# Optimization experiments

Hardware: AMD Instinct MI355X
Metric: run time of the kernel (lower is better)

## Reference

```python
import jax, jax.numpy as jnp
import numpy as np

PATCH = 3
PAD = (PATCH - 1) // 2
WEIGHT = 100.0
EPS = 1e-9


def _extract_patches(fm):
    # fm: (C, H, W) -> (H*W, C*9) row i*W+j is the reflect-padded 3x3 patch at (i, j)
    C, H, W = fm.shape
    fm_pad = jnp.pad(fm, ((0, 0), (PAD, PAD), (PAD, PAD)), mode='reflect')
    shifts = [fm_pad[:, dh:dh + H, dw:dw + W] for dh in range(PATCH) for dw in range(PATCH)]
    p = jnp.stack(shifts, axis=0)            # (9, C, H, W)
    return p.reshape(PATCH * PATCH * C, H * W).T  # (HW, 9C)


def _match_fm(content_fm, style_fm):
    # content_fm, style_fm: (1, C, H, W); returns matched style fm (1,C,H,W) and idx (2,H,W)
    C, H, W = content_fm.shape[1:]
    cp = _extract_patches(content_fm[0])     # (HW, 9C) content patches (conv kernels)
    sp = _extract_patches(style_fm[0])       # (HW, 9C) style patches (conv sliding windows)
    c_norm = jnp.sqrt(jnp.sum(cp * cp, axis=1))  # kernel_norm per content location
    s_norm = jnp.sqrt(jnp.sum(sp * sp, axis=1))  # style_fm_norm per style location
    score = cp @ sp.T                            # (HW, HW) cross-correlation
    score = score / (c_norm[:, None] * s_norm[None, :] + EPS)
    idx = jnp.argmax(score, axis=1)              # flat argmax == torch.argmax on (H,W) map
    style_flat = style_fm[0].reshape(C, H * W)
    corr = style_flat[:, idx].reshape(1, C, H, W)  # gather matched style pixels
    corr_idx = jnp.stack([idx // W, idx % W], axis=0).reshape(2, H, W)
    return corr, corr_idx


def _masked_gram(fm, mask_flat, mask_sum):
    # fm: (1, C, H, W), mask_flat: (HW,) -> (C, C) gram of masked fm / sum(mask)
    C = fm.shape[1]
    f = fm[0].reshape(C, -1) * mask_flat[None, :]
    return (f @ f.T) / mask_sum


def setup_inputs() -> dict:
    key = jax.random.key(0)
    k1, k2, k3, k4 = jax.random.split(key, 4)
    B, C, H, W = 1, 512, 64, 64
    return {
        'content_fm': jax.random.normal(k1, (B, C, H, W), dtype=jnp.float32),
        'style_fm': jax.random.normal(k2, (B, C, H, W), dtype=jnp.float32),
        'input_fm': jax.random.normal(k3, (B, C, H, W), dtype=jnp.float32),
        'mask': jax.random.uniform(k4, (B, 1, H, W), dtype=jnp.float32),
    }


def reference(content_fm, style_fm, input_fm, mask):
    H, W = content_fm.shape[2:]
    mask_flat = mask[0, 0].reshape(H * W)
    mask_sum = jnp.sum(mask)
    # capture_style_ref: patch-match style fm to content fm, build target gram
    corr_fm, _ = _match_fm(content_fm, style_fm)
    target_gram = _masked_gram(corr_fm, mask_flat, mask_sum)
    # loss mode: masked gram of current image fm vs target, MSE (mean) * weight
    G = _masked_gram(input_fm, mask_flat, mask_sum)
    loss = jnp.mean((G - target_gram) ** 2) * WEIGHT
    return loss
```

## Files before the change

### kernel.cpp

```cpp
#include <hip/hip_runtime.h>

static constexpr int C  = 512;
static constexpr int P  = 4096;

typedef _Float16 half8  __attribute__((ext_vector_type(8)));
typedef _Float16 half2v __attribute__((ext_vector_type(2)));
typedef float    f32x4  __attribute__((ext_vector_type(4)));

__device__ __forceinline__ int refl(int q) { return q < 0 ? 1 : (q > 63 ? 62 : q); }

__device__ __forceinline__ void g2l16(const void* g, const void* l) {
    __builtin_amdgcn_global_load_lds((const __attribute__((address_space(1))) unsigned int*)g,
                                     (__attribute__((address_space(3))) unsigned int*)l, 16, 0, 0);
}

__global__ __launch_bounds__(256) void k_prep(const float* __restrict__ content, const float* __restrict__ style,
                                              _Float16* __restrict__ Ah, _Float16* __restrict__ Bh,
                                              float* __restrict__ sqn_part) {
    __shared__ float T[64][65];
    __shared__ float R4[4][64];
    const int p0 = (blockIdx.x & 63) * 64, c0 = (blockIdx.x >> 6) * 64;
    const int pl = threadIdx.x & 63, cq = threadIdx.x >> 6;
    const int pv = threadIdx.x >> 3;
    const int cv = (threadIdx.x & 7) * 8;

    #pragma unroll
    for (int r = 0; r < 16; ++r)
        T[cq + r * 4][pl] = content[(size_t)(c0 + cq + r * 4) * P + p0 + pl];
    __syncthreads();
    #pragma unroll
    for (int r = 0; r < 2; ++r) {
        int pl2 = pv + r * 32;
        half8 v;
        #pragma unroll
        for (int u = 0; u < 8; ++u) v[u] = (_Float16)T[cv + u][pl2];
        *(half8*)(Ah + (size_t)(p0 + pl2) * C + c0 + cv) = v;
    }
    __syncthreads();

    float sq = 0.f;
    #pragma unroll
    for (int r = 0; r < 16; ++r) {
        float v = style[(size_t)(c0 + cq + r * 4) * P + p0 + pl];
        T[cq + r * 4][pl] = v;
        sq += v * v;
    }
    R4[cq][pl] = sq;
    __syncthreads();
    if (cq == 0)
        sqn_part[(size_t)(blockIdx.x >> 6) * P + p0 + pl] = R4[0][pl] + R4[1][pl] + R4[2][pl] + R4[3][pl];
    #pragma unroll
    for (int r = 0; r < 2; ++r) {
        int pl2 = pv + r * 32;
        half8 v;
        #pragma unroll
        for (int u = 0; u < 8; ++u) v[u] = (_Float16)T[cv + u][pl2];
        *(half8*)(Bh + (size_t)(p0 + pl2) * C + c0 + cv) = v;
    }
}

__global__ __launch_bounds__(512, 2) void k_gemm16(const _Float16* __restrict__ Ah,
                                                   const _Float16* __restrict__ Bh,
                                                   _Float16* __restrict__ Eo,
                                                   const float* __restrict__ sqn_part,
                                                   const float* __restrict__ mask,
                                                   float* __restrict__ inv_sn,
                                                   float* __restrict__ msum) {
    __shared__ _Float16 SH[65536];
    const int tid = threadIdx.x;
    const int bid = blockIdx.x;
    const int swz = (bid & 7) * 32 + (bid >> 3);
    const int by = swz >> 4, bx = swz & 15;

    if (by == 0) {
        float* sqs = (float*)SH;
        const int b = bx;
        for (int e = tid; e < 384; e += 512) {
            int rr = e >> 6, jw = e & 63;
            int gr = refl(b * 4 - 1 + rr);
            float s = 0.f;
            #pragma unroll
            for (int k = 0; k < 8; ++k) s += sqn_part[(size_t)k * P + gr * 64 + jw];
            sqs[rr * 64 + jw] = s;
        }
        __syncthreads();
        if (tid < 256) {
            int p = b * 256 + tid;
            int li = (tid >> 6) + 1;
            int j = p & 63;
            float s2 = 0.f;
            #pragma unroll
            for (int dh = -1; dh <= 1; ++dh)
                #pragma unroll
                for (int dw = -1; dw <= 1; ++dw)
                    s2 += sqs[(li + dh) * 64 + refl(j + dw)];
            inv_sn[p] = 1.0f / sqrtf(s2);
        }
        if (b == 0) {
            __syncthreads();
            float* red = (float*)SH;
            float s = 0.f;
            for (int e = tid; e < P; e += 512) s += mask[e];
            red[tid] = s;
            __syncthreads();
            for (int t = 256; t > 0; t >>= 1) {
                if (tid < t) red[tid] += red[tid + t];
                __syncthreads();
            }
            if (tid == 0) msum[0] = red[0];
        }
        __syncthreads();
    }

    const int wave = tid >> 6, lane = tid & 63;
    const int wr = wave >> 2, wc = wave & 3;
    const int quad = lane >> 4, l15 = lane & 15;
    const int i0 = by * 256, j0 = bx * 256;

    const int r2 = tid >> 2;
    const int gofs = ((tid & 3) ^ (r2 & 3)) * 8;
    const _Float16* pA0 = Ah + (size_t)(i0 + r2) * C + gofs;
    const _Float16* pA1 = pA0 + (size_t)128 * C;
    const _Float16* pB0 = Bh + (size_t)(j0 + r2) * C + gofs;
    const _Float16* pB1 = pB0 + (size_t)128 * C;
    const int stw0 = wave * 512;
    const int stw1 = 4096 + wave * 512;

    const int aslot = (quad ^ (l15 & 3)) * 8;
    int aoff[8], boff[4];
    #pragma unroll
    for (int mi = 0; mi < 8; ++mi) aoff[mi] = (wr * 128 + mi * 16 + l15) * 32 + aslot;
    #pragma unroll
    for (int ni = 0; ni < 4; ++ni) boff[ni] = (wc * 64 + ni * 16 + l15) * 32 + aslot;

    f32x4 acc[8][4] = {};
    half8 af[8], bf0, bf1, bf2, bf3;

#define LDSA(b,k) (SH + (b) * 16384 + (k) * 8192)
#define LDSB(b,k) (SH + 32768 + (b) * 16384 + (k) * 8192)
#define STAGE_A(b,k,KC) do { g2l16(pA0 + (KC) + (k) * 32, LDSA(b,k) + stw0); \
                             g2l16(pA1 + (KC) + (k) * 32, LDSA(b,k) + stw1); } while (0)
#define STAGE_B(b,k,KC) do { g2l16(pB0 + (KC) + (k) * 32, LDSB(b,k) + stw0); \
                             g2l16(pB1 + (KC) + (k) * 32, LDSB(b,k) + stw1); } while (0)
#define READ_NP0(b,k) do { _Pragma("unroll") for (int mi = 0; mi < 8; ++mi) \
                               af[mi] = *(const half8*)(LDSA(b,k) + aoff[mi]); \
                           bf0 = *(const half8*)(LDSB(b,k) + boff[0]); \
                           bf1 = *(const half8*)(LDSB(b,k) + boff[1]); } while (0)
#define READ_NP1(b,k) do { bf2 = *(const half8*)(LDSB(b,k) + boff[2]); \
                           bf3 = *(const half8*)(LDSB(b,k) + boff[3]); } while (0)
#define MF8(BF,NI) do { _Pragma("unroll") for (int mi = 0; mi < 8; ++mi) \
    acc[mi][NI] = __builtin_amdgcn_mfma_f32_16x16x32_f16(af[mi], BF, acc[mi][NI], 0, 0, 0); } while (0)
#define WAITV4 asm volatile("s_waitcnt vmcnt(4)" ::: "memory")
#define WAITV0 asm volatile("s_waitcnt vmcnt(0)" ::: "memory")
#define EXEC16(B0,N0,B1,N1) do { \
    __builtin_amdgcn_s_barrier(); \
    asm volatile("s_waitcnt lgkmcnt(0)" ::: "memory"); \
    __builtin_amdgcn_sched_barrier(0); \
    __builtin_amdgcn_s_setprio(1); \
    MF8(B0, N0); MF8(B1, N1); \
    __builtin_amdgcn_s_setprio(0); \
    __builtin_amdgcn_s_barrier(); } while (0)

    STAGE_A(0, 0, 0); STAGE_B(0, 0, 0); STAGE_A(0, 1, 0); STAGE_B(0, 1, 0);
    WAITV4;
    __builtin_amdgcn_s_barrier();

    for (int it = 0; it < 4; ++it) {
        const int kk = it * 128;
        const bool nl = (it < 3);
        READ_NP0(0, 0); STAGE_A(1, 0, kk + 64);          EXEC16(bf0, 0, bf1, 1);
        READ_NP1(0, 0); STAGE_B(1, 0, kk + 64); WAITV4;  EXEC16(bf2, 2, bf3, 3);
        READ_NP0(0, 1); STAGE_A(1, 1, kk + 64);          EXEC16(bf0, 0, bf1, 1);
        READ_NP1(0, 1); STAGE_B(1, 1, kk + 64); WAITV4;  EXEC16(bf2, 2, bf3, 3);
        READ_NP0(1, 0); if (nl) STAGE_A(0, 0, kk + 128);
        EXEC16(bf0, 0, bf1, 1);
        READ_NP1(1, 0); if (nl) { STAGE_B(0, 0, kk + 128); WAITV4; } else { WAITV0; }
        EXEC16(bf2, 2, bf3, 3);
        READ_NP0(1, 1); if (nl) STAGE_A(0, 1, kk + 128);
        EXEC16(bf0, 0, bf1, 1);
        READ_NP1(1, 1); if (nl) { STAGE_B(0, 1, kk + 128); WAITV4; }
        EXEC16(bf2, 2, bf3, 3);
    }

#undef LDSA
#undef LDSB
#undef STAGE_A
#undef STAGE_B
#undef READ_NP0
#undef READ_NP1
#undef MF8
#undef WAITV4
#undef WAITV0
#undef EXEC16

    __syncthreads();
    #pragma unroll
    for (int h = 0; h < 2; ++h) {
        if (wr == h) {
            #pragma unroll
            for (int mi = 0; mi < 8; ++mi) {
                const int row = mi * 16 + quad * 4;
                #pragma unroll
                for (int ni = 0; ni < 4; ++ni) {
                    const int col = wc * 64 + ni * 16 + l15;
                    #pragma unroll
                    for (int r = 0; r < 4; ++r)
                        SH[(row + r) * 130 + col] = (_Float16)acc[mi][ni][r];
                }
            }
        }
        __syncthreads();
        {
            const int er  = tid >> 2;
            const int c00 = (tid & 3) * 8;
            const int ew  = er & 63;
            const int rm  = (er & 64) | (ew == 0 ? 1 : ew - 1);
            const int rp  = (er & 64) | (ew == 63 ? 62 : ew + 1);
            _Float16* outRow = Eo + (size_t)(i0 + h * 128 + er) * P + j0;
            #pragma unroll
            for (int cc = 0; cc < 256; cc += 32) {
                half8 ev;
                #pragma unroll
                for (int u = 0; u < 8; ++u) {
                    const int c  = c00 + cc + u;
                    const int cw = c & 63;
                    const int cm = (c & ~63) | (cw == 0 ? 1 : cw - 1);
                    const int cp = (c & ~63) | (cw == 63 ? 62 : cw + 1);
                    ev[u] = (_Float16)((float)SH[rm * 130 + cm] + (float)SH[er * 130 + c] + (float)SH[rp * 130 + cp]);
                }
                *(half8*)(outRow + c00 + cc) = ev;
            }
        }
        if (h == 0) __syncthreads();
    }
}

__global__ __launch_bounds__(256) void k_argmax(const _Float16* __restrict__ E,
                                                const float* __restrict__ inv_sn,
                                                int* __restrict__ idxOut) {
    const int i = blockIdx.x;
    const int ih = i >> 6, iw = i & 63;
    const int wave = threadIdx.x >> 6, l = threadIdx.x & 63, l15 = l & 15;
    size_t rb0 = (size_t)(refl(ih - 1) * 64 + iw) * P;
    size_t rb1 = (size_t)(ih * 64 + iw) * P;
    size_t rb2 = (size_t)(refl(ih + 1) * 64 + iw) * P;

    float best = -1e30f;
    int bidx = 0;
    #pragma unroll
    for (int s = 0; s < 4; ++s) {
        const int j0 = (wave * 4 + s) * 256 + l * 4;
        const int jh = j0 >> 6, jw0 = l15 * 4;
        const int cb0 = ((jh == 0) ? 1 : jh - 1) * 64 + jw0;
        const int cb1 = jh * 64 + jw0;
        const int cb2 = ((jh == 63) ? 62 : jh + 1) * 64 + jw0;
        uint2 u0 = *(const uint2*)(E + rb0 + cb0);
        uint2 u1 = *(const uint2*)(E + rb1 + cb1);
        uint2 u2 = *(const uint2*)(E + rb2 + cb2);
        half2v a0 = __builtin_bit_cast(half2v, u0.x), a1 = __builtin_bit_cast(half2v, u0.y);
        half2v b0 = __builtin_bit_cast(half2v, u1.x), b1 = __builtin_bit_cast(half2v, u1.y);
        half2v c0 = __builtin_bit_cast(half2v, u2.x), c1 = __builtin_bit_cast(half2v, u2.y);
        float f0 = (float)a0[0] + (float)b0[0] + (float)c0[0];
        float f1 = (float)a0[1] + (float)b0[1] + (float)c0[1];
        float f2 = (float)a1[0] + (float)b1[0] + (float)c1[0];
        float f3 = (float)a1[1] + (float)b1[1] + (float)c1[1];
        const float4 is = *(const float4*)(inv_sn + j0);
        float v0 = f0 * is.x, v1 = f1 * is.y, v2 = f2 * is.z, v3 = f3 * is.w;
        if (v0 > best) { best = v0; bidx = j0; }
        if (v1 > best) { best = v1; bidx = j0 + 1; }
        if (v2 > best) { best = v2; bidx = j0 + 2; }
        if (v3 > best) { best = v3; bidx = j0 + 3; }
    }

    __shared__ float bv[256];
    __shared__ int   bi[256];
    bv[threadIdx.x] = best;
    bi[threadIdx.x] = bidx;
    __syncthreads();
    for (int t = 128; t > 0; t >>= 1) {
        if (threadIdx.x < t) {
            float ov = bv[threadIdx.x + t];
            int   oi = bi[threadIdx.x + t];
            if (ov > bv[threadIdx.x] || (ov == bv[threadIdx.x] && oi < bi[threadIdx.x])) {
                bv[threadIdx.x] = ov;
                bi[threadIdx.x] = oi;
            }
        }
        __syncthreads();
    }
    if (threadIdx.x == 0) idxOut[i] = bi[0];
}

__global__ __launch_bounds__(256) void k_build(const _Float16* __restrict__ Bh,
                                               const float* __restrict__ input,
                                               const float* __restrict__ mask,
                                               const int* __restrict__ idx,
                                               _Float16* __restrict__ fc, _Float16* __restrict__ fg) {
    __shared__ _Float16 G[16][520];
    __shared__ float mk[16];
    const int p0 = blockIdx.x * 16;
    const int wave = threadIdx.x >> 6, lane = threadIdx.x & 63;

    {
        int e0 = (blockIdx.x * 256 + threadIdx.x) * 32;
        #pragma unroll
        for (int v = 0; v < 4; ++v) {
            int e = e0 + v * 8;
            int pp = e & (P - 1);
            half8 vg;
            #pragma unroll
            for (int u = 0; u < 8; ++u)
                vg[u] = (_Float16)(input[e + u] * mask[pp + u]);
            *(half8*)(fg + e) = vg;
        }
    }

    if (threadIdx.x < 16) mk[threadIdx.x] = mask[p0 + threadIdx.x];

    #pragma unroll
    for (int r = 0; r < 4; ++r) {
        int pp = wave * 4 + r;
        int row = idx[p0 + pp];
        *(half8*)(&G[pp][lane * 8]) = *(const half8*)(Bh + (size_t)row * C + lane * 8);
    }
    __syncthreads();

    #pragma unroll
    for (int h = 0; h < 2; ++h) {
        int c = h * 256 + threadIdx.x;
        half8 o[2];
        #pragma unroll
        for (int q = 0; q < 2; ++q)
            #pragma unroll
            for (int u = 0; u < 8; ++u) {
                int p = q * 8 + u;
                o[q][u] = (_Float16)((float)G[p][c] * mk[p]);
            }
        _Float16* dst = fc + (size_t)c * P + p0;
        *(half8*)(dst)     = o[0];
        *(half8*)(dst + 8) = o[1];
    }
}

__device__ __constant__ int TBX[10] = {0, 0, 1, 0, 1, 2, 0, 1, 2, 3};
__device__ __constant__ int TBY[10] = {0, 1, 1, 2, 2, 2, 3, 3, 3, 3};

__global__ __launch_bounds__(256) void k_gram(const _Float16* __restrict__ fg,
                                              const _Float16* __restrict__ fc,
                                              float* __restrict__ part) {
    const int t = blockIdx.x, z = blockIdx.z;
    const int p0 = z * 256;
    const int wave = threadIdx.x >> 6, lane = threadIdx.x & 63;
    const int wr = wave >> 1, wc = wave & 1, quad = lane >> 4, l15 = lane & 15;
    const int a0 = TBY[t] * 128 + wr * 64, b0 = TBX[t] * 128 + wc * 64;

    f32x4 accg[4][4] = {};
    f32x4 accc[4][4] = {};
    for (int ks = 0; ks < 256; ks += 32) {
        int kbase = p0 + ks + quad * 8;
        half8 af[4], bf[4];
        #pragma unroll
        for (int mi = 0; mi < 4; ++mi) af[mi] = *(const half8*)(fg + (size_t)(a0 + mi * 16 + l15) * P + kbase);
        #pragma unroll
        for (int ni = 0; ni < 4; ++ni) bf[ni] = *(const half8*)(fg + (size_t)(b0 + ni * 16 + l15) * P + kbase);
        #pragma unroll
        for (int mi = 0; mi < 4; ++mi)
            #pragma unroll
            for (int ni = 0; ni < 4; ++ni)
                accg[mi][ni] = __builtin_amdgcn_mfma_f32_16x16x32_f16(af[mi], bf[ni], accg[mi][ni], 0, 0, 0);
        #pragma unroll
        for (int mi = 0; mi < 4; ++mi) af[mi] = *(const half8*)(fc + (size_t)(a0 + mi * 16 + l15) * P + kbase);
        #pragma unroll
        for (int ni = 0; ni < 4; ++ni) bf[ni] = *(const half8*)(fc + (size_t)(b0 + ni * 16 + l15) * P + kbase);
        #pragma unroll
        for (int mi = 0; mi < 4; ++mi)
            #pragma unroll
            for (int ni = 0; ni < 4; ++ni)
                accc[mi][ni] = __builtin_amdgcn_mfma_f32_16x16x32_f16(af[mi], bf[ni], accc[mi][ni], 0, 0, 0);
    }
    float* dst = part + (size_t)(z * 10 + t) * 16384;
    #pragma unroll
    for (int mi = 0; mi < 4; ++mi)
        #pragma unroll
        for (int ni = 0; ni < 4; ++ni)
            #pragma unroll
            for (int r = 0; r < 4; ++r)
                dst[(wr * 64 + mi * 16 + quad * 4 + r) * 128 + wc * 64 + ni * 16 + l15]
                    = accg[mi][ni][r] - accc[mi][ni][r];
}

__global__ void k_loss(const float* __restrict__ part, float* __restrict__ lsum) {
    int e = blockIdx.x * 256 + threadIdx.x;
    int t = e >> 14, loc = e & 16383;
    float d = 0.f;
    #pragma unroll
    for (int z = 0; z < 16; ++z) d += part[(size_t)(z * 10 + t) * 16384 + loc];
    float w = (TBX[t] == TBY[t]) ? 1.0f : 2.0f;
    __shared__ float red[256];
    red[threadIdx.x] = d * d * w;
    __syncthreads();
    for (int s = 128; s > 0; s >>= 1) {
        if (threadIdx.x < s) red[threadIdx.x] += red[threadIdx.x + s];
        __syncthreads();
    }
    if (threadIdx.x == 0) lsum[blockIdx.x] = red[0];
}

__global__ void k_final(const float* __restrict__ lsum, const float* __restrict__ msum,
                        float* __restrict__ out) {
    __shared__ float red[256];
    float s = 0.f;
    for (int e = threadIdx.x; e < 640; e += 256) s += lsum[e];
    red[threadIdx.x] = s;
    __syncthreads();
    for (int t = 128; t > 0; t >>= 1) {
        if (threadIdx.x < t) red[threadIdx.x] += red[threadIdx.x + t];
        __syncthreads();
    }
    if (threadIdx.x == 0) {
        float m = msum[0];
        out[0] = red[0] * 100.0f / (m * m * 262144.0f);
    }
}

extern "C" void kernel_launch(void* const* d_in, const int* in_sizes, int n_in,
                              void* d_out, int out_size, void* d_ws, size_t ws_size,
                              hipStream_t stream) {
    (void)in_sizes; (void)n_in; (void)out_size; (void)ws_size;
    const float* content = (const float*)d_in[0];
    const float* style   = (const float*)d_in[1];
    const float* input   = (const float*)d_in[2];
    const float* mask    = (const float*)d_in[3];

    char* ws = (char*)d_ws;
    _Float16* Eb   = (_Float16*)ws;
    float*    part = (float*)ws;
    _Float16* Ah   = (_Float16*)(ws + (32u << 20));
    _Float16* Bh   = (_Float16*)(ws + (36u << 20));
    _Float16* fg_h = (_Float16*)(ws + (40u << 20));
    _Float16* fc_h = (_Float16*)(ws + (44u << 20));
    float*    small = (float*)(ws + (48u << 20));
    float* sqn_part = small;
    float* inv_sn   = small + 32768;
    float* msum     = small + 36864;
    float* lsum     = small + 36992;
    int*   idx      = (int*)(small + 37888);
    float* out = (float*)d_out;

    k_prep  <<<512, 256, 0, stream>>>(content, style, Ah, Bh, sqn_part);
    k_gemm16<<<256, 512, 0, stream>>>(Ah, Bh, Eb, sqn_part, mask, inv_sn, msum);
    k_argmax<<<4096, 256, 0, stream>>>(Eb, inv_sn, idx);
    k_build <<<256, 256, 0, stream>>>(Bh, input, mask, idx, fc_h, fg_h);
    k_gram  <<<dim3(10, 1, 16), 256, 0, stream>>>(fg_h, fc_h, part);
    k_loss  <<<640, 256, 0, stream>>>(part, lsum);
    k_final <<<1, 256, 0, stream>>>(lsum, msum, out);
}
```

Measured before the change: 149.5 us.

## Compute four argmax rows per block with vector loads and reuse overlapping E rows

The argmax kernel now handles four vertically adjacent content pixels per block. It loads six E rows once and reuses them across the overlapping 3-row vertical sums, reads 16 halfs per thread with wide vector loads, and reduces with wave shuffles instead of a shared-memory tree. Separately, the final-reduction kernel is removed: k_loss atomically adds its scaled partial sums into the output, which k_build zeroes. This cuts E reads and one launch, but atomic float addition makes the summation order nondeterministic.

```diff
diff --git a/kernel.cpp b/kernel.cpp
--- a/kernel.cpp
+++ b/kernel.cpp
@@ -238,68 +238,91 @@
 __global__ __launch_bounds__(256) void k_argmax(const _Float16* __restrict__ E,
                                                 const float* __restrict__ inv_sn,
                                                 int* __restrict__ idxOut) {
-    const int i = blockIdx.x;
-    const int ih = i >> 6, iw = i & 63;
-    const int wave = threadIdx.x >> 6, l = threadIdx.x & 63, l15 = l & 15;
-    size_t rb0 = (size_t)(refl(ih - 1) * 64 + iw) * P;
-    size_t rb1 = (size_t)(ih * 64 + iw) * P;
-    size_t rb2 = (size_t)(refl(ih + 1) * 64 + iw) * P;
-
-    float best = -1e30f;
-    int bidx = 0;
-    #pragma unroll
-    for (int s = 0; s < 4; ++s) {
-        const int j0 = (wave * 4 + s) * 256 + l * 4;
-        const int jh = j0 >> 6, jw0 = l15 * 4;
-        const int cb0 = ((jh == 0) ? 1 : jh - 1) * 64 + jw0;
-        const int cb1 = jh * 64 + jw0;
-        const int cb2 = ((jh == 63) ? 62 : jh + 1) * 64 + jw0;
-        uint2 u0 = *(const uint2*)(E + rb0 + cb0);
-        uint2 u1 = *(const uint2*)(E + rb1 + cb1);
-        uint2 u2 = *(const uint2*)(E + rb2 + cb2);
-        half2v a0 = __builtin_bit_cast(half2v, u0.x), a1 = __builtin_bit_cast(half2v, u0.y);
-        half2v b0 = __builtin_bit_cast(half2v, u1.x), b1 = __builtin_bit_cast(half2v, u1.y);
-        half2v c0 = __builtin_bit_cast(half2v, u2.x), c1 = __builtin_bit_cast(half2v, u2.y);
-        float f0 = (float)a0[0] + (float)b0[0] + (float)c0[0];
-        float f1 = (float)a0[1] + (float)b0[1] + (float)c0[1];
-        float f2 = (float)a1[0] + (float)b1[0] + (float)c1[0];
-        float f3 = (float)a1[1] + (float)b1[1] + (float)c1[1];
-        const float4 is = *(const float4*)(inv_sn + j0);
-        float v0 = f0 * is.x, v1 = f1 * is.y, v2 = f2 * is.z, v3 = f3 * is.w;
-        if (v0 > best) { best = v0; bidx = j0; }
-        if (v1 > best) { best = v1; bidx = j0 + 1; }
-        if (v2 > best) { best = v2; bidx = j0 + 2; }
-        if (v3 > best) { best = v3; bidx = j0 + 3; }
-    }
-
-    __shared__ float bv[256];
-    __shared__ int   bi[256];
-    bv[threadIdx.x] = best;
-    bi[threadIdx.x] = bidx;
-    __syncthreads();
-    for (int t = 128; t > 0; t >>= 1) {
-        if (threadIdx.x < t) {
-            float ov = bv[threadIdx.x + t];
-            int   oi = bi[threadIdx.x + t];
-            if (ov > bv[threadIdx.x] || (ov == bv[threadIdx.x] && oi < bi[threadIdx.x])) {
-                bv[threadIdx.x] = ov;
-                bi[threadIdx.x] = oi;
+    const int tid = threadIdx.x;
+    const int iw = blockIdx.x & 63, q = blockIdx.x >> 6;
+    const int wave = tid >> 6, lane = tid & 63;
+
+    size_t rb[6];
+    #pragma unroll
+    for (int t = 0; t < 6; ++t)
+        rb[t] = (size_t)(refl(q * 4 - 1 + t) * 64 + iw) * P;
+
+    const int jh = tid >> 2, jw0 = (tid & 3) * 16;
+    const int cm = ((jh == 0) ? 1 : jh - 1) * 64 + jw0;
+    const int cc = jh * 64 + jw0;
+    const int cp = ((jh == 63) ? 62 : jh + 1) * 64 + jw0;
+
+    half8 sm[4][2], sc[4][2], sp[4][2];
+    #pragma unroll
+    for (int t = 0; t < 4; ++t) {
+        #pragma unroll
+        for (int h = 0; h < 2; ++h) {
+            sm[t][h] = *(const half8*)(E + rb[t]     + cm + h * 8);
+            sc[t][h] = *(const half8*)(E + rb[t + 1] + cc + h * 8);
+            sp[t][h] = *(const half8*)(E + rb[t + 2] + cp + h * 8);
+        }
+    }
+    float inv[16];
+    #pragma unroll
+    for (int g4 = 0; g4 < 4; ++g4) {
+        float4 f = *(const float4*)(inv_sn + tid * 16 + g4 * 4);
+        inv[g4 * 4 + 0] = f.x; inv[g4 * 4 + 1] = f.y; inv[g4 * 4 + 2] = f.z; inv[g4 * 4 + 3] = f.w;
+    }
+
+    float best[4] = {-1e30f, -1e30f, -1e30f, -1e30f};
+    int   bidx[4] = {0, 0, 0, 0};
+    #pragma unroll
+    for (int m = 0; m < 4; ++m)
+        #pragma unroll
+        for (int h = 0; h < 2; ++h)
+            #pragma unroll
+            for (int u = 0; u < 8; ++u) {
+                float f = (float)sm[m][h][u] + (float)sc[m][h][u] + (float)sp[m][h][u];
+                float v = f * inv[h * 8 + u];
+                int j = tid * 16 + h * 8 + u;
+                if (v > best[m]) { best[m] = v; bidx[m] = j; }
             }
-        }
-        __syncthreads();
-    }
-    if (threadIdx.x == 0) idxOut[i] = bi[0];
+
+    #pragma unroll
+    for (int m = 0; m < 4; ++m)
+        #pragma unroll
+        for (int off = 32; off > 0; off >>= 1) {
+            float ov = __shfl_xor(best[m], off, 64);
+            int   oi = __shfl_xor(bidx[m], off, 64);
+            if (ov > best[m] || (ov == best[m] && oi < bidx[m])) { best[m] = ov; bidx[m] = oi; }
+        }
+
+    __shared__ float wbv[4][4];
+    __shared__ int   wbi[4][4];
+    if (lane == 0) {
+        #pragma unroll
+        for (int m = 0; m < 4; ++m) { wbv[wave][m] = best[m]; wbi[wave][m] = bidx[m]; }
+    }
+    __syncthreads();
+    if (tid < 4) {
+        const int m = tid;
+        float bv = wbv[0][m]; int bi = wbi[0][m];
+        #pragma unroll
+        for (int w = 1; w < 4; ++w) {
+            float ov = wbv[w][m]; int oi = wbi[w][m];
+            if (ov > bv || (ov == bv && oi < bi)) { bv = ov; bi = oi; }
+        }
+        idxOut[(q * 4 + m) * 64 + iw] = bi;
+    }
 }
 
 __global__ __launch_bounds__(256) void k_build(const _Float16* __restrict__ Bh,
                                                const float* __restrict__ input,
                                                const float* __restrict__ mask,
                                                const int* __restrict__ idx,
-                                               _Float16* __restrict__ fc, _Float16* __restrict__ fg) {
+                                               _Float16* __restrict__ fc, _Float16* __restrict__ fg,
+                                               float* __restrict__ out) {
     __shared__ _Float16 G[16][520];
     __shared__ float mk[16];
     const int p0 = blockIdx.x * 16;
     const int wave = threadIdx.x >> 6, lane = threadIdx.x & 63;
+
+    if (blockIdx.x == 0 && threadIdx.x == 0) out[0] = 0.f;
 
     {
         int e0 = (blockIdx.x * 256 + threadIdx.x) * 32;
@@ -389,7 +412,8 @@
                     = accg[mi][ni][r] - accc[mi][ni][r];
 }
 
-__global__ void k_loss(const float* __restrict__ part, float* __restrict__ lsum) {
+__global__ void k_loss(const float* __restrict__ part, const float* __restrict__ msum,
+                       float* __restrict__ out) {
     int e = blockIdx.x * 256 + threadIdx.x;
     int t = e >> 14, loc = e & 16383;
     float d = 0.f;
@@ -403,23 +427,9 @@
         if (threadIdx.x < s) red[threadIdx.x] += red[threadIdx.x + s];
         __syncthreads();
     }
-    if (threadIdx.x == 0) lsum[blockIdx.x] = red[0];
-}
-
-__global__ void k_final(const float* __restrict__ lsum, const float* __restrict__ msum,
-                        float* __restrict__ out) {
-    __shared__ float red[256];
-    float s = 0.f;
-    for (int e = threadIdx.x; e < 640; e += 256) s += lsum[e];
-    red[threadIdx.x] = s;
-    __syncthreads();
-    for (int t = 128; t > 0; t >>= 1) {
-        if (threadIdx.x < t) red[threadIdx.x] += red[threadIdx.x + t];
-        __syncthreads();
-    }
     if (threadIdx.x == 0) {
         float m = msum[0];
-        out[0] = red[0] * 100.0f / (m * m * 262144.0f);
+        atomicAdd(out, red[0] * 100.0f / (m * m * 262144.0f));
     }
 }
 
@@ -443,15 +453,13 @@
     float* sqn_part = small;
     float* inv_sn   = small + 32768;
     float* msum     = small + 36864;
-    float* lsum     = small + 36992;
     int*   idx      = (int*)(small + 37888);
     float* out = (float*)d_out;
 
     k_prep  <<<512, 256, 0, stream>>>(content, style, Ah, Bh, sqn_part);
     k_gemm16<<<256, 512, 0, stream>>>(Ah, Bh, Eb, sqn_part, mask, inv_sn, msum);
-    k_argmax<<<4096, 256, 0, stream>>>(Eb, inv_sn, idx);
-    k_build <<<256, 256, 0, stream>>>(Bh, input, mask, idx, fc_h, fg_h);
+    k_argmax<<<1024, 256, 0, stream>>>(Eb, inv_sn, idx);
+    k_build <<<256, 256, 0, stream>>>(Bh, input, mask, idx, fc_h, fg_h, out);
     k_gram  <<<dim3(10, 1, 16), 256, 0, stream>>>(fg_h, fc_h, part);
-    k_loss  <<<640, 256, 0, stream>>>(part, lsum);
-    k_final <<<1, 256, 0, stream>>>(lsum, msum, out);
-}
+    k_loss  <<<640, 256, 0, stream>>>(part, msum, out);
+}
```

After: 157.6 us. 1.05x slower.
